# Kernel optimization log

Measured on AMD Instinct MI355X. Metric: run time of the kernel, lower is better.

The kernel has to match this reference:

```python
import jax, jax.numpy as jnp
import numpy as np

N, D = 4096, 512
TAU, ALPHA, EPS = 0.2, 0.5, 1e-15
L2_EPS = 1e-12  # F.normalize eps


def setup_inputs() -> dict:
    key = jax.random.key(0)
    ks = jax.random.split(key, 12)
    # xavier_normal_ with gain=1.414 for [D, D] linears
    std = 1.414 * (2.0 / (D + D)) ** 0.5
    xn = lambda k: jax.random.normal(k, (D, D), jnp.float32) * std
    return {
        "z1": jax.random.normal(ks[0], (N, D), jnp.float32),
        "z2": jax.random.normal(ks[1], (N, D), jnp.float32),
        # local projector: Linear -> PReLU -> Linear
        "lw1": xn(ks[2]), "lb1": jnp.zeros((D,), jnp.float32),
        "la": jnp.full((1,), 0.25, jnp.float32),  # PReLU weight (torch default 0.25)
        "lw2": xn(ks[3]), "lb2": jnp.zeros((D,), jnp.float32),
        # global projector
        "gw1": xn(ks[4]), "gb1": jnp.zeros((D,), jnp.float32),
        "ga": jnp.full((1,), 0.25, jnp.float32),
        "gw2": xn(ks[5]), "gb2": jnp.zeros((D,), jnp.float32),
        # discriminator bilinear weight
        "W": xn(ks[6]),
        # binary positive-pair mask [N, N]
        "mask": jax.random.randint(ks[7], (N, N), 0, 2, jnp.int32),
    }


def _prelu(x, a):
    return jnp.where(x >= 0, x, a * x)


def _proj(z, w1, b1, a, w2, b2):
    # nn.Sequential(Linear, PReLU, Linear); torch Linear: z @ W.T + b
    return _prelu(z @ w1.T + b1, a[0]) @ w2.T + b2


def _l2norm(z):
    n = jnp.linalg.norm(z, axis=-1, keepdims=True)
    return z / jnp.maximum(n, L2_EPS)


def _infonce(h1, h2, m, tau):
    a = _l2norm(h1)
    b = _l2norm(h2)
    sim_intra = jnp.exp(a @ a.T / tau)  # [N, N]
    sim_inter = jnp.exp(a @ b.T / tau)  # [N, N]
    num = (sim_inter * m).sum(1)
    den = sim_intra.sum(1) + sim_inter.sum(1) - (sim_intra * m).sum(1)
    return (-jnp.log(num / den)).mean()


def reference(z1, z2, lw1, lb1, la, lw2, lb2, gw1, gb1, ga, gw2, gb2, W, mask):
    m = mask.astype(jnp.float32)
    # local (node-level) InfoNCE through the local projector
    h1 = _proj(z1, lw1, lb1, la, lw2, lb2)
    h2 = _proj(z2, lw1, lb1, la, lw2, lb2)
    local = 0.5 * (_infonce(h1, h2, m, TAU) + _infonce(h2, h1, m.T, TAU))

    # global (DGI-style) loss
    def gloss(pos_z, neg_z):
        s = pos_z.mean(0)                               # readout [D]
        h = _proj(s, gw1, gb1, ga, gw2, gb2)            # global projector [D]
        summ = W @ h                                    # [D]
        d_pos = jax.nn.sigmoid(pos_z @ summ)            # [N]
        d_neg = jax.nn.sigmoid(neg_z @ summ)            # [N]
        pos_loss = -jnp.log(d_pos + EPS).mean()
        neg_loss = -jnp.log(1.0 - d_neg + EPS).mean()
        return 0.5 * (pos_loss + neg_loss)

    glob = 0.5 * (gloss(z1, z2) + gloss(z2, z1))
    return ALPHA * local + (1.0 - ALPHA) * glob
```

## Files before the change

### kernel.cpp

```cpp
#include <hip/hip_runtime.h>
#include <math.h>

#define NN 4096
#define DD 512
#define INV_TAU 5.0f
#define EPSV 1e-15f

typedef unsigned short u16;
typedef __attribute__((ext_vector_type(8))) short short8;
typedef __attribute__((ext_vector_type(4))) float f32x4;

__device__ __forceinline__ void gld16(const void* g, void* l) {
  __builtin_amdgcn_global_load_lds(
      (const __attribute__((address_space(1))) unsigned int*)g,
      (__attribute__((address_space(3))) unsigned int*)l, 16, 0, 0);
}

__device__ __forceinline__ void bar_vm4() {
  asm volatile("s_waitcnt vmcnt(4) lgkmcnt(0)\n\ts_barrier" ::: "memory");
}
__device__ __forceinline__ void bar_vm0() {
  asm volatile("s_waitcnt vmcnt(0) lgkmcnt(0)\n\ts_barrier" ::: "memory");
}

__device__ __forceinline__ float bf2f(u16 u) {
  return __uint_as_float(((unsigned)u) << 16);
}
__device__ __forceinline__ u16 f2bf(float x) {
  unsigned u = __float_as_uint(x);
  u += 0x7fff + ((u >> 16) & 1);
  return (u16)(u >> 16);
}

__device__ __forceinline__ float wave_sum(float v) {
#pragma unroll
  for (int o = 32; o > 0; o >>= 1) v += __shfl_down(v, o, 64);
  return v;
}

__global__ __launch_bounds__(256) void tobf16_2(const float* __restrict__ a,
                                                const float* __restrict__ b,
                                                u16* __restrict__ d,
                                                int n4each) {
  const int i = blockIdx.x * 256 + threadIdx.x;
  const float* s =
      (i < n4each) ? a + (size_t)i * 4 : b + (size_t)(i - n4each) * 4;
  float4 v = *(const float4*)s;
  unsigned long long pk = (unsigned long long)f2bf(v.x) |
                          ((unsigned long long)f2bf(v.y) << 16) |
                          ((unsigned long long)f2bf(v.z) << 32) |
                          ((unsigned long long)f2bf(v.w) << 48);
  *(unsigned long long*)&d[(size_t)i * 4] = pk;
}

template <int ACT>
__global__ __launch_bounds__(256) void gemm_mfma(
    const u16* __restrict__ A, const u16* __restrict__ Bw,
    const float* __restrict__ bias, const float* __restrict__ alpha_p,
    u16* __restrict__ out) {
  __shared__ __align__(16) u16 sh[3 * 2 * 128 * 32];
  const int tid = threadIdx.x, w = tid >> 6, lane = tid & 63;
  const int quad = lane >> 4, m16 = lane & 15;
  const int wi = w >> 1, wj = w & 1;
  const int i0 = blockIdx.y * 128, j0 = blockIdx.x * 128;
  const u16* Ab = A + (size_t)blockIdx.z * ((size_t)NN * DD);
  u16* ob = out + (size_t)blockIdx.z * ((size_t)NN * DD);
  const int roff =
      (m16 >> 1) * 64 + (((((m16 & 1) << 2) | quad) ^ (m16 >> 1)) * 8);
  const int st = (lane & 7) ^ (lane >> 3);
  const int srow = 2 * (lane >> 3) + (st >> 2);
  const int scol = (st & 3) * 8;
  const int p = w >> 1, rh = (w & 1) * 64;
  const u16* gs = p ? Bw : Ab;
  const int gr = (p ? j0 : i0) + rh + srow;
  u16* dst0 = sh + p * 4096 + rh * 32;
  auto stage = [&](int bo, int k) {
    const int kn = k * 32;
#pragma unroll
    for (int rr = 0; rr < 64; rr += 16)
      gld16(&gs[(size_t)(gr + rr) * DD + kn + scol], dst0 + bo + rr * 32);
  };
  stage(0, 0);
  stage(8192, 1);
  bar_vm4();
  f32x4 acc[4][4] = {};
  int ro = 0;
  for (int kc = 0; kc < 16; ++kc) {
    if (kc <= 13) {
      int so = ro + 16384;
      if (so >= 24576) so -= 24576;
      stage(so, kc + 2);
    }
    const u16* As = sh + ro;
    const u16* Bs = sh + ro + 4096;
    short8 ar[4], br[4];
#pragma unroll
    for (int s = 0; s < 4; ++s) {
      ar[s] = *(const short8*)&As[(wi * 64 + s * 16) * 32 + roff];
      br[s] = *(const short8*)&Bs[(wj * 64 + s * 16) * 32 + roff];
    }
    __builtin_amdgcn_s_setprio(1);
#pragma unroll
    for (int si = 0; si < 4; ++si)
#pragma unroll
      for (int sj = 0; sj < 4; ++sj)
        acc[si][sj] = __builtin_amdgcn_mfma_f32_16x16x32_bf16(
            ar[si], br[sj], acc[si][sj], 0, 0, 0);
    __builtin_amdgcn_s_setprio(0);
    if (kc <= 13) bar_vm4();
    else if (kc == 14) bar_vm0();
    ro += 8192;
    if (ro == 24576) ro = 0;
  }
  const float al = ACT ? alpha_p[0] : 0.f;
#pragma unroll
  for (int si = 0; si < 4; ++si)
#pragma unroll
    for (int sj = 0; sj < 4; ++sj) {
      const int col = j0 + wj * 64 + sj * 16 + m16;
      const float bv = bias[col];
#pragma unroll
      for (int r = 0; r < 4; ++r) {
        const int row = i0 + wi * 64 + si * 16 + quad * 4 + r;
        float x = acc[si][sj][r] + bv;
        if (ACT) x = (x >= 0.f) ? x : al * x;
        ob[(size_t)row * DD + col] = f2bf(x);
      }
    }
}

__global__ __launch_bounds__(256) void rownorm_bf16(const u16* __restrict__ h,
                                                    u16* __restrict__ o) {
  const int row = blockIdx.x;
  const int t = threadIdx.x;
  const size_t base = (size_t)row * DD;
  float v0 = bf2f(h[base + t]);
  float v1 = bf2f(h[base + 256 + t]);
  float s = v0 * v0 + v1 * v1;
  s = wave_sum(s);
  __shared__ float wsum[4];
  const int lane = t & 63, wid = t >> 6;
  if (lane == 0) wsum[wid] = s;
  __syncthreads();
  if (t == 0) {
    float tot = wsum[0] + wsum[1] + wsum[2] + wsum[3];
    wsum[0] = 1.f / fmaxf(sqrtf(tot), 1e-12f);
  }
  __syncthreads();
  const float inv = wsum[0];
  o[base + t] = f2bf(v0 * inv);
  o[base + 256 + t] = f2bf(v1 * inv);
}

__global__ __launch_bounds__(512) void sim_mfma(
    const u16* __restrict__ na, const u16* __restrict__ nb,
    const int* __restrict__ mask, float* __restrict__ zb) {
  extern __shared__ __align__(16) u16 shm[];
  const int tid = threadIdx.x;
  const int w = tid >> 6, lane = tid & 63;
  const int quad = lane >> 4, m16 = lane & 15;
  const int ig = w & 3, jh = w >> 2;
  const int i0 = blockIdx.y * 128, j0 = blockIdx.x * 128;
  const int roff =
      (m16 >> 1) * 64 + (((((m16 & 1) << 2) | quad) ^ (m16 >> 1)) * 8);
  const int st = (lane & 7) ^ (lane >> 3);
  const int srow = 2 * (lane >> 3) + (st >> 2);
  const int scol = (st & 3) * 8;
  const int p = w >> 1, rh = (w & 1) * 64;
  const u16* gs = (p & 1) ? nb : na;
  const int gr = ((p < 2) ? i0 : j0) + rh + srow;
  u16* dst0 = shm + p * 4096 + rh * 32;
  auto stage = [&](int bo, int k) {
    const int kn = k * 32;
#pragma unroll
    for (int rr = 0; rr < 64; rr += 16)
      gld16(&gs[(size_t)(gr + rr) * DD + kn + scol], dst0 + bo + rr * 32);
  };
  stage(0, 0);
  stage(16384, 1);
  bar_vm4();
  f32x4 a11[2][4] = {}, a12[2][4] = {}, a22[2][4] = {};
  int ro = 0;
  for (int kc = 0; kc < 16; ++kc) {
    if (kc <= 13) {
      int so = ro + 32768;
      if (so >= 49152) so -= 49152;
      stage(so, kc + 2);
    }
    const u16* Ai = shm + ro;
    const u16* Bi = shm + ro + 4096;
    const u16* Aj = shm + ro + 8192;
    const u16* Bj = shm + ro + 12288;
    short8 ai0 = *(const short8*)&Ai[(ig * 32) * 32 + roff];
    short8 ai1 = *(const short8*)&Ai[(ig * 32 + 16) * 32 + roff];
    short8 bi0 = *(const short8*)&Bi[(ig * 32) * 32 + roff];
    short8 bi1 = *(const short8*)&Bi[(ig * 32 + 16) * 32 + roff];
#pragma unroll
    for (int c = 0; c < 4; ++c) {
      short8 aj = *(const short8*)&Aj[(jh * 64 + c * 16) * 32 + roff];
      short8 bj = *(const short8*)&Bj[(jh * 64 + c * 16) * 32 + roff];
      __builtin_amdgcn_s_setprio(1);
      a11[0][c] = __builtin_amdgcn_mfma_f32_16x16x32_bf16(ai0, aj, a11[0][c], 0, 0, 0);
      a11[1][c] = __builtin_amdgcn_mfma_f32_16x16x32_bf16(ai1, aj, a11[1][c], 0, 0, 0);
      a12[0][c] = __builtin_amdgcn_mfma_f32_16x16x32_bf16(ai0, bj, a12[0][c], 0, 0, 0);
      a12[1][c] = __builtin_amdgcn_mfma_f32_16x16x32_bf16(ai1, bj, a12[1][c], 0, 0, 0);
      a22[0][c] = __builtin_amdgcn_mfma_f32_16x16x32_bf16(bi0, bj, a22[0][c], 0, 0, 0);
      a22[1][c] = __builtin_amdgcn_mfma_f32_16x16x32_bf16(bi1, bj, a22[1][c], 0, 0, 0);
      __builtin_amdgcn_s_setprio(0);
    }
    if (kc <= 13) bar_vm4();
    else if (kc == 14) bar_vm0();
    ro += 16384;
    if (ro == 49152) ro = 0;
  }
  float* rred = (float*)(shm + 16384);
  float* cred = rred + 512;
  rred[tid] = 0.f;
  rred[tid + 512] = 0.f;
  __syncthreads();
  float rs11[2][4] = {}, rm11[2][4] = {}, rs12[2][4] = {}, rm12[2][4] = {};
  float cs12[4] = {}, cm12[4] = {}, cs22[4] = {}, cm22[4] = {};
#pragma unroll
  for (int t = 0; t < 2; ++t)
#pragma unroll
    for (int c = 0; c < 4; ++c) {
      const int gj = j0 + jh * 64 + c * 16 + m16;
#pragma unroll
      for (int r = 0; r < 4; ++r) {
        const int gi = i0 + ig * 32 + t * 16 + quad * 4 + r;
        const float mv = (float)mask[(size_t)gi * NN + gj];
        const float e11 = __expf(a11[t][c][r] * INV_TAU);
        const float e12 = __expf(a12[t][c][r] * INV_TAU);
        const float e22 = __expf(a22[t][c][r] * INV_TAU);
        rs11[t][r] += e11;
        rm11[t][r] += e11 * mv;
        rs12[t][r] += e12;
        rm12[t][r] += e12 * mv;
        cs12[c] += e12;
        cm12[c] += e12 * mv;
        cs22[c] += e22;
        cm22[c] += e22 * mv;
      }
    }
#pragma unroll
  for (int t = 0; t < 2; ++t)
#pragma unroll
    for (int r = 0; r < 4; ++r) {
      float v0 = rs11[t][r], v1 = rm11[t][r], v2 = rs12[t][r], v3 = rm12[t][r];
#pragma unroll
      for (int o = 1; o < 16; o <<= 1) {
        v0 += __shfl_xor(v0, o, 64);
        v1 += __shfl_xor(v1, o, 64);
        v2 += __shfl_xor(v2, o, 64);
        v3 += __shfl_xor(v3, o, 64);
      }
      if (m16 == 0) {
        const int il = ig * 32 + t * 16 + quad * 4 + r;
        atomicAdd(&rred[0 * 128 + il], v0);
        atomicAdd(&rred[1 * 128 + il], v1);
        atomicAdd(&rred[2 * 128 + il], v2);
        atomicAdd(&rred[3 * 128 + il], v3);
      }
    }
#pragma unroll
  for (int c = 0; c < 4; ++c) {
    float v0 = cs12[c], v1 = cm12[c], v2 = cs22[c], v3 = cm22[c];
    v0 += __shfl_xor(v0, 16, 64); v0 += __shfl_xor(v0, 32, 64);
    v1 += __shfl_xor(v1, 16, 64); v1 += __shfl_xor(v1, 32, 64);
    v2 += __shfl_xor(v2, 16, 64); v2 += __shfl_xor(v2, 32, 64);
    v3 += __shfl_xor(v3, 16, 64); v3 += __shfl_xor(v3, 32, 64);
    if (lane < 16) {
      const int jl = jh * 64 + c * 16 + lane;
      atomicAdd(&cred[0 * 128 + jl], v0);
      atomicAdd(&cred[1 * 128 + jl], v1);
      atomicAdd(&cred[2 * 128 + jl], v2);
      atomicAdd(&cred[3 * 128 + jl], v3);
    }
  }
  __syncthreads();
  if (tid < 128) {
#pragma unroll
    for (int q = 0; q < 4; ++q)
      atomicAdd(&zb[q * NN + i0 + tid], rred[q * 128 + tid]);
  } else if (tid < 256) {
    const int jl = tid - 128;
#pragma unroll
    for (int q = 0; q < 4; ++q)
      atomicAdd(&zb[(4 + q) * NN + j0 + jl], cred[q * 128 + jl]);
  }
}

__global__ __launch_bounds__(256) void local_fin(const float* __restrict__ zb,
                                                 float* __restrict__ scal) {
  const int i = blockIdx.x * 256 + threadIdx.x;
  const float r11 = zb[i], r11m = zb[NN + i];
  const float r12 = zb[2 * NN + i], r12m = zb[3 * NN + i];
  const float c12 = zb[4 * NN + i], c12m = zb[5 * NN + i];
  const float c22 = zb[6 * NN + i], c22m = zb[7 * NN + i];
  float l1 = -logf(r12m / (r11 + r12 - r11m));
  float l2 = -logf(c12m / (c22 + c12 - c22m));
  l1 = wave_sum(l1);
  l2 = wave_sum(l2);
  __shared__ float b1[4], b2[4];
  const int lane = threadIdx.x & 63, wid = threadIdx.x >> 6;
  if (lane == 0) { b1[wid] = l1; b2[wid] = l2; }
  __syncthreads();
  if (threadIdx.x == 0) {
    atomicAdd(&scal[0], b1[0] + b1[1] + b1[2] + b1[3]);
    atomicAdd(&scal[1], b2[0] + b2[1] + b2[2] + b2[3]);
  }
}

__global__ __launch_bounds__(256) void colmean(const float* __restrict__ z1,
                                               const float* __restrict__ z2,
                                               float* __restrict__ s1,
                                               float* __restrict__ s2) {
  const int c = blockIdx.x * 256 + threadIdx.x;
  const int r0 = blockIdx.y * 64;
  float a = 0.f, b = 0.f;
  for (int r = r0; r < r0 + 64; ++r) {
    a += z1[(size_t)r * DD + c];
    b += z2[(size_t)r * DD + c];
  }
  atomicAdd(&s1[c], a * (1.f / NN));
  atomicAdd(&s2[c], b * (1.f / NN));
}

__global__ __launch_bounds__(256) void matvec2(
    const float* __restrict__ M, const float* __restrict__ x1,
    const float* __restrict__ x2, const float* __restrict__ bias,
    const float* __restrict__ alpha_p, int act, float* __restrict__ y1,
    float* __restrict__ y2) {
  const float* x = blockIdx.y ? x2 : x1;
  float* y = blockIdx.y ? y2 : y1;
  const int row = (blockIdx.x * 256 + threadIdx.x) >> 6;
  const int lane = threadIdx.x & 63;
  float acc = 0.f;
#pragma unroll
  for (int t = 0; t < 8; ++t)
    acc = fmaf(M[(size_t)row * DD + lane + 64 * t], x[lane + 64 * t], acc);
  acc = wave_sum(acc);
  if (lane == 0) {
    if (bias) acc += bias[row];
    if (act) { const float al = alpha_p[0]; acc = (acc >= 0.f) ? acc : al * acc; }
    y[row] = acc;
  }
}

__global__ __launch_bounds__(256) void logsig2(
    const float* __restrict__ z1, const float* __restrict__ z2,
    const float* __restrict__ sm1, const float* __restrict__ sm2,
    float* __restrict__ scal) {
  const int ch = blockIdx.y;
  const float* z = ch ? z2 : z1;
  const float* sp = ch ? sm2 : sm1;
  const float* sn = ch ? sm1 : sm2;
  float* accP = ch ? &scal[4] : &scal[2];
  float* accN = ch ? &scal[3] : &scal[5];
  const int lane = threadIdx.x & 63;
  const int wid = threadIdx.x >> 6;
  const int row = blockIdx.x * 4 + wid;
  float dp = 0.f, dn = 0.f;
#pragma unroll
  for (int t = 0; t < 8; ++t) {
    const float zv = z[(size_t)row * DD + lane + 64 * t];
    dp = fmaf(zv, sp[lane + 64 * t], dp);
    dn = fmaf(zv, sn[lane + 64 * t], dn);
  }
  dp = wave_sum(dp);
  dn = wave_sum(dn);
  __shared__ float bp[4], bn[4];
  if (lane == 0) {
    const float sg = 1.f / (1.f + __expf(-dp));
    bp[wid] = -logf(sg + EPSV);
    const float sg2 = 1.f / (1.f + __expf(-dn));
    bn[wid] = -logf(1.f - sg2 + EPSV);
  }
  __syncthreads();
  if (threadIdx.x == 0) {
    atomicAdd(accP, bp[0] + bp[1] + bp[2] + bp[3]);
    atomicAdd(accN, bn[0] + bn[1] + bn[2] + bn[3]);
  }
}

__global__ void combine(const float* __restrict__ scal, float* __restrict__ out) {
  const float local = 0.5f * (scal[0] + scal[1]) * (1.f / NN);
  const float glob = 0.25f * (scal[2] + scal[3] + scal[4] + scal[5]) * (1.f / NN);
  out[0] = 0.5f * local + 0.5f * glob;
}

extern "C" void kernel_launch(void* const* d_in, const int* in_sizes, int n_in,
                              void* d_out, int out_size, void* d_ws,
                              size_t ws_size, hipStream_t stream) {
  const float* z1 = (const float*)d_in[0];
  const float* z2 = (const float*)d_in[1];
  const float* lw1 = (const float*)d_in[2];
  const float* lb1 = (const float*)d_in[3];
  const float* la = (const float*)d_in[4];
  const float* lw2 = (const float*)d_in[5];
  const float* lb2 = (const float*)d_in[6];
  const float* gw1 = (const float*)d_in[7];
  const float* gb1 = (const float*)d_in[8];
  const float* ga = (const float*)d_in[9];
  const float* gw2 = (const float*)d_in[10];
  const float* gb2 = (const float*)d_in[11];
  const float* W = (const float*)d_in[12];
  const int* mask = (const int*)d_in[13];
  float* out = (float*)d_out;

  static bool attr_set = false;
  if (!attr_set) {
    (void)hipFuncSetAttribute(reinterpret_cast<const void*>(sim_mfma),
                              hipFuncAttributeMaxDynamicSharedMemorySize,
                              98304);
    attr_set = true;
  }

  const size_t ND = (size_t)NN * DD;
  u16* W1b = (u16*)d_ws;
  u16* W2b = W1b + 512 * 512;
  u16* Ab = W1b + 2 * 512 * 512;
  u16* Bb = Ab + 2 * ND;
  float* zbf = (float*)(Bb + 2 * ND);
  float* s1 = zbf + 8 * NN;
  float* s2 = s1 + DD;
  float* scal = s2 + DD;
  float* t1 = scal + 16;
  float* hg1 = t1 + DD;
  float* summ1 = hg1 + DD;
  float* t2 = summ1 + DD;
  float* hg2 = t2 + DD;
  float* summ2 = hg2 + DD;

  hipMemsetAsync(zbf, 0, (8 * NN + 2 * DD + 16) * sizeof(float), stream);

  dim3 blk(256);
  tobf16_2<<<512, blk, 0, stream>>>(lw1, lw2, W1b, 512 * 512 / 4);
  tobf16_2<<<4096, blk, 0, stream>>>(z1, z2, Ab, (int)(ND / 4));

  dim3 gg(4, 32, 2);
  gemm_mfma<1><<<gg, blk, 0, stream>>>(Ab, W1b, lb1, la, Bb);
  gemm_mfma<0><<<gg, blk, 0, stream>>>(Bb, W2b, lb2, la, Ab);
  rownorm_bf16<<<2 * NN, blk, 0, stream>>>(Ab, Bb);

  sim_mfma<<<dim3(NN / 128, NN / 128), dim3(512), 98304, stream>>>(
      Bb, Bb + ND, mask, zbf);
  local_fin<<<NN / 256, blk, 0, stream>>>(zbf, scal);

  colmean<<<dim3(DD / 256, 64), blk, 0, stream>>>(z1, z2, s1, s2);
  matvec2<<<dim3(DD / 4, 2), blk, 0, stream>>>(gw1, s1, s2, gb1, ga, 1, t1, t2);
  matvec2<<<dim3(DD / 4, 2), blk, 0, stream>>>(gw2, t1, t2, gb2, nullptr, 0, hg1, hg2);
  matvec2<<<dim3(DD / 4, 2), blk, 0, stream>>>(W, hg1, hg2, nullptr, nullptr, 0, summ1, summ2);
  logsig2<<<dim3(NN / 4, 2), blk, 0, stream>>>(z1, z2, summ1, summ2, scal);

  combine<<<1, 1, 0, stream>>>(scal, out);
}
```

Before: 310.2 us.

## Fuse pipeline: merged conversion/colsum, GEMM+rownorm, single matvec chain, last-block finalize

Replaces most of the launch sequence. The bf16 conversion of weights and z, the zeroing of accumulators and the column partial sums now run in one kernel. The first GEMM gets a 512-thread, XCD-aware 128x64 tiling, and the second GEMM is fused with L2 row normalization over full-width 32-row bands. The three global matvecs become one 2-block kernel, and the loss finalize and combine run in the last sim_mfma block via an atomic counter. This removes the memset, several launches and intermediate round-trips through memory, at the cost of a serial single-block tail and low parallelism in mv_chain.

```diff
diff --git a/kernel.cpp b/kernel.cpp
--- a/kernel.cpp
+++ b/kernel.cpp
@@ -16,8 +16,17 @@
       (__attribute__((address_space(3))) unsigned int*)l, 16, 0, 0);
 }
 
+__device__ __forceinline__ void bar_vm5() {
+  asm volatile("s_waitcnt vmcnt(5) lgkmcnt(0)\n\ts_barrier" ::: "memory");
+}
 __device__ __forceinline__ void bar_vm4() {
   asm volatile("s_waitcnt vmcnt(4) lgkmcnt(0)\n\ts_barrier" ::: "memory");
+}
+__device__ __forceinline__ void bar_vm2() {
+  asm volatile("s_waitcnt vmcnt(2) lgkmcnt(0)\n\ts_barrier" ::: "memory");
+}
+__device__ __forceinline__ void bar_vm1() {
+  asm volatile("s_waitcnt vmcnt(1) lgkmcnt(0)\n\ts_barrier" ::: "memory");
 }
 __device__ __forceinline__ void bar_vm0() {
   asm volatile("s_waitcnt vmcnt(0) lgkmcnt(0)\n\ts_barrier" ::: "memory");
@@ -38,123 +47,382 @@
   return v;
 }
 
-__global__ __launch_bounds__(256) void tobf16_2(const float* __restrict__ a,
-                                                const float* __restrict__ b,
-                                                u16* __restrict__ d,
-                                                int n4each) {
-  const int i = blockIdx.x * 256 + threadIdx.x;
-  const float* s =
-      (i < n4each) ? a + (size_t)i * 4 : b + (size_t)(i - n4each) * 4;
+__device__ __forceinline__ float ldz(const float* p) {
+  return __hip_atomic_load(p, __ATOMIC_RELAXED, __HIP_MEMORY_SCOPE_AGENT);
+}
+
+__global__ __launch_bounds__(256) void tobf16cm(
+    const float* __restrict__ a, const float* __restrict__ b,
+    const float* __restrict__ c, const float* __restrict__ d2,
+    u16* __restrict__ o, float* __restrict__ pc1, float* __restrict__ pc2,
+    float* __restrict__ zbf, int* __restrict__ ctr) {
+  const int bid = blockIdx.x, tid = threadIdx.x;
+  if (bid >= 4608) {
+    const int blk = bid - 4608;
+    const int r0 = blk * 32;
+    float a0 = 0.f, a1 = 0.f, c0 = 0.f, c1 = 0.f;
+    for (int r = r0; r < r0 + 32; ++r) {
+      const size_t ro = (size_t)r * DD;
+      a0 += c[ro + tid];
+      a1 += c[ro + 256 + tid];
+      c0 += d2[ro + tid];
+      c1 += d2[ro + 256 + tid];
+    }
+    pc1[blk * 512 + tid] = a0;
+    pc1[blk * 512 + 256 + tid] = a1;
+    pc2[blk * 512 + tid] = c0;
+    pc2[blk * 512 + 256 + tid] = c1;
+    return;
+  }
+  if (bid == 0 && tid == 0) ctr[0] = 0;
+  if (bid < 128) zbf[bid * 256 + tid] = 0.f;
+  const int i = bid * 256 + tid;
+  int j = i;
+  const float* s;
+  if (j < 65536) {
+    s = a + (size_t)j * 4;
+  } else {
+    j -= 65536;
+    if (j < 65536) {
+      s = b + (size_t)j * 4;
+    } else {
+      j -= 65536;
+      if (j < 524288) {
+        s = c + (size_t)j * 4;
+      } else {
+        j -= 524288;
+        s = d2 + (size_t)j * 4;
+      }
+    }
+  }
   float4 v = *(const float4*)s;
   unsigned long long pk = (unsigned long long)f2bf(v.x) |
                           ((unsigned long long)f2bf(v.y) << 16) |
                           ((unsigned long long)f2bf(v.z) << 32) |
                           ((unsigned long long)f2bf(v.w) << 48);
-  *(unsigned long long*)&d[(size_t)i * 4] = pk;
+  *(unsigned long long*)&o[(size_t)i * 4] = pk;
 }
 
 template <int ACT>
-__global__ __launch_bounds__(256) void gemm_mfma(
+__global__ __launch_bounds__(512) void gemm_mfma(
     const u16* __restrict__ A, const u16* __restrict__ Bw,
     const float* __restrict__ bias, const float* __restrict__ alpha_p,
     u16* __restrict__ out) {
-  __shared__ __align__(16) u16 sh[3 * 2 * 128 * 32];
+  __shared__ __align__(16) u16 sh[3 * 6144];
   const int tid = threadIdx.x, w = tid >> 6, lane = tid & 63;
   const int quad = lane >> 4, m16 = lane & 15;
   const int wi = w >> 1, wj = w & 1;
-  const int i0 = blockIdx.y * 128, j0 = blockIdx.x * 128;
-  const u16* Ab = A + (size_t)blockIdx.z * ((size_t)NN * DD);
-  u16* ob = out + (size_t)blockIdx.z * ((size_t)NN * DD);
+  const int bid = blockIdx.x;
+  const int xcd = bid & 7, idx = bid >> 3;
+  const int i0 = (4 * xcd + (idx & 3)) * 128;
+  const int j0 = ((idx >> 2) & 7) * 64;
+  const int bz = idx >> 5;
+  const u16* Ab = A + (size_t)bz * ((size_t)NN * DD);
+  u16* ob = out + (size_t)bz * ((size_t)NN * DD);
   const int roff =
       (m16 >> 1) * 64 + (((((m16 & 1) << 2) | quad) ^ (m16 >> 1)) * 8);
   const int st = (lane & 7) ^ (lane >> 3);
   const int srow = 2 * (lane >> 3) + (st >> 2);
   const int scol = (st & 3) * 8;
-  const int p = w >> 1, rh = (w & 1) * 64;
-  const u16* gs = p ? Bw : Ab;
-  const int gr = (p ? j0 : i0) + rh + srow;
-  u16* dst0 = sh + p * 4096 + rh * 32;
+  const u16* gs = (w < 4) ? Ab : Bw;
+  const int grow0 = ((w < 4) ? i0 + 2 * w * 16 : j0 + (w - 4) * 16) + srow;
+  const int doff0 = (w < 4) ? 2 * w * 512 : 4096 + (w - 4) * 512;
   auto stage = [&](int bo, int k) {
     const int kn = k * 32;
-#pragma unroll
-    for (int rr = 0; rr < 64; rr += 16)
-      gld16(&gs[(size_t)(gr + rr) * DD + kn + scol], dst0 + bo + rr * 32);
+    gld16(&gs[(size_t)grow0 * DD + kn + scol], sh + bo + doff0);
+    if (w < 4)
+      gld16(&gs[(size_t)(grow0 + 16) * DD + kn + scol], sh + bo + doff0 + 512);
   };
   stage(0, 0);
-  stage(8192, 1);
-  bar_vm4();
-  f32x4 acc[4][4] = {};
+  stage(6144, 1);
+  if (w < 4) bar_vm2(); else bar_vm1();
+  f32x4 acc[2][2] = {};
   int ro = 0;
   for (int kc = 0; kc < 16; ++kc) {
     if (kc <= 13) {
-      int so = ro + 16384;
-      if (so >= 24576) so -= 24576;
+      int so = ro + 12288;
+      if (so >= 18432) so -= 18432;
       stage(so, kc + 2);
     }
     const u16* As = sh + ro;
     const u16* Bs = sh + ro + 4096;
-    short8 ar[4], br[4];
-#pragma unroll
-    for (int s = 0; s < 4; ++s) {
-      ar[s] = *(const short8*)&As[(wi * 64 + s * 16) * 32 + roff];
-      br[s] = *(const short8*)&Bs[(wj * 64 + s * 16) * 32 + roff];
+    short8 ar[2], br[2];
+#pragma unroll
+    for (int s = 0; s < 2; ++s) {
+      ar[s] = *(const short8*)&As[(wi * 32 + s * 16) * 32 + roff];
+      br[s] = *(const short8*)&Bs[(wj * 32 + s * 16) * 32 + roff];
     }
     __builtin_amdgcn_s_setprio(1);
 #pragma unroll
-    for (int si = 0; si < 4; ++si)
+    for (int si = 0; si < 2; ++si)
+#pragma unroll
+      for (int sj = 0; sj < 2; ++sj)
+        acc[si][sj] = __builtin_amdgcn_mfma_f32_16x16x32_bf16(
+            ar[si], br[sj], acc[si][sj], 0, 0, 0);
+    __builtin_amdgcn_s_setprio(0);
+    if (kc <= 13) {
+      if (w < 4) bar_vm2(); else bar_vm1();
+    } else if (kc == 14) {
+      bar_vm0();
+    }
+    ro += 6144;
+    if (ro == 18432) ro = 0;
+  }
+  const float al = ACT ? alpha_p[0] : 0.f;
+#pragma unroll
+  for (int si = 0; si < 2; ++si)
+#pragma unroll
+    for (int sj = 0; sj < 2; ++sj) {
+      const int col = j0 + wj * 32 + sj * 16 + m16;
+      const float bv = bias[col];
+#pragma unroll
+      for (int r = 0; r < 4; ++r) {
+        const int row = i0 + wi * 32 + si * 16 + quad * 4 + r;
+        float x = acc[si][sj][r] + bv;
+        if (ACT) x = (x >= 0.f) ? x : al * x;
+        ob[(size_t)row * DD + col] = f2bf(x);
+      }
+    }
+}
+
+__global__ __launch_bounds__(512) void gemm2n(const u16* __restrict__ Ain,
+                                              const u16* __restrict__ Bw,
+                                              const float* __restrict__ bias,
+                                              u16* __restrict__ outn) {
+  extern __shared__ __align__(16) u16 shb[];
+  const int BUF = 17408;
+  const int tid = threadIdx.x, w = tid >> 6, lane = tid & 63;
+  const int quad = lane >> 4, m16 = lane & 15;
+  const int bid = blockIdx.x;
+  const int bz = bid >> 7, band = bid & 127;
+  const int i0 = band * 32;
+  const u16* Ab = Ain + (size_t)bz * ((size_t)NN * DD);
+  u16* ob = outn + (size_t)bz * ((size_t)NN * DD);
+  const int roff =
+      (m16 >> 1) * 64 + (((((m16 & 1) << 2) | quad) ^ (m16 >> 1)) * 8);
+  const int st = (lane & 7) ^ (lane >> 3);
+  const int srow = 2 * (lane >> 3) + (st >> 2);
+  const int scol = (st & 3) * 8;
+  const int g0 = w * 4;
+  auto stage = [&](int bo, int k) {
+    const int kn = k * 32;
+#pragma unroll
+    for (int q = 0; q < 4; ++q) {
+      const int grow = (g0 + q) * 16 + srow;
+      gld16(&Bw[(size_t)grow * DD + kn + scol], shb + bo + (g0 + q) * 512);
+    }
+    if (w < 2) {
+      const int grow = i0 + w * 16 + srow;
+      gld16(&Ab[(size_t)grow * DD + kn + scol], shb + bo + 16384 + w * 512);
+    }
+  };
+  stage(0, 0);
+  stage(BUF, 1);
+  if (w < 2) bar_vm5(); else bar_vm4();
+  f32x4 acc[2][4] = {};
+  int ro = 0;
+  for (int kc = 0; kc < 16; ++kc) {
+    if (kc <= 13) {
+      int so = ro + 2 * BUF;
+      if (so >= 3 * BUF) so -= 3 * BUF;
+      stage(so, kc + 2);
+    }
+    const u16* Bs = shb + ro;
+    const u16* As = shb + ro + 16384;
+    short8 ar[2], br[4];
+#pragma unroll
+    for (int s = 0; s < 2; ++s)
+      ar[s] = *(const short8*)&As[(s * 16) * 32 + roff];
+#pragma unroll
+    for (int s = 0; s < 4; ++s)
+      br[s] = *(const short8*)&Bs[(w * 64 + s * 16) * 32 + roff];
+    __builtin_amdgcn_s_setprio(1);
+#pragma unroll
+    for (int si = 0; si < 2; ++si)
 #pragma unroll
       for (int sj = 0; sj < 4; ++sj)
         acc[si][sj] = __builtin_amdgcn_mfma_f32_16x16x32_bf16(
             ar[si], br[sj], acc[si][sj], 0, 0, 0);
     __builtin_amdgcn_s_setprio(0);
-    if (kc <= 13) bar_vm4();
-    else if (kc == 14) bar_vm0();
-    ro += 8192;
-    if (ro == 24576) ro = 0;
-  }
-  const float al = ACT ? alpha_p[0] : 0.f;
-#pragma unroll
-  for (int si = 0; si < 4; ++si)
+    if (kc <= 13) {
+      if (w < 2) bar_vm5(); else bar_vm4();
+    } else if (kc == 14) {
+      bar_vm0();
+    }
+    ro += BUF;
+    if (ro == 3 * BUF) ro = 0;
+  }
+  float ss[2][4] = {};
+#pragma unroll
+  for (int si = 0; si < 2; ++si)
 #pragma unroll
     for (int sj = 0; sj < 4; ++sj) {
-      const int col = j0 + wj * 64 + sj * 16 + m16;
-      const float bv = bias[col];
+      const float bv = bias[w * 64 + sj * 16 + m16];
 #pragma unroll
       for (int r = 0; r < 4; ++r) {
-        const int row = i0 + wi * 64 + si * 16 + quad * 4 + r;
-        float x = acc[si][sj][r] + bv;
-        if (ACT) x = (x >= 0.f) ? x : al * x;
-        ob[(size_t)row * DD + col] = f2bf(x);
+        const float x = acc[si][sj][r] + bv;
+        acc[si][sj][r] = x;
+        ss[si][r] = fmaf(x, x, ss[si][r]);
       }
     }
-}
-
-__global__ __launch_bounds__(256) void rownorm_bf16(const u16* __restrict__ h,
-                                                    u16* __restrict__ o) {
-  const int row = blockIdx.x;
-  const int t = threadIdx.x;
-  const size_t base = (size_t)row * DD;
-  float v0 = bf2f(h[base + t]);
-  float v1 = bf2f(h[base + 256 + t]);
-  float s = v0 * v0 + v1 * v1;
-  s = wave_sum(s);
-  __shared__ float wsum[4];
-  const int lane = t & 63, wid = t >> 6;
-  if (lane == 0) wsum[wid] = s;
-  __syncthreads();
-  if (t == 0) {
-    float tot = wsum[0] + wsum[1] + wsum[2] + wsum[3];
-    wsum[0] = 1.f / fmaxf(sqrtf(tot), 1e-12f);
-  }
-  __syncthreads();
-  const float inv = wsum[0];
-  o[base + t] = f2bf(v0 * inv);
-  o[base + 256 + t] = f2bf(v1 * inv);
+#pragma unroll
+  for (int si = 0; si < 2; ++si)
+#pragma unroll
+    for (int r = 0; r < 4; ++r) {
+#pragma unroll
+      for (int o = 1; o < 16; o <<= 1) ss[si][r] += __shfl_xor(ss[si][r], o, 64);
+    }
+  float* part = (float*)(shb + BUF);
+  float* invn = part + 256;
+  if (m16 == 0) {
+#pragma unroll
+    for (int si = 0; si < 2; ++si)
+#pragma unroll
+      for (int r = 0; r < 4; ++r)
+        part[(si * 16 + quad * 4 + r) * 8 + w] = ss[si][r];
+  }
+  __syncthreads();
+  if (tid < 32) {
+    float s = 0.f;
+#pragma unroll
+    for (int q = 0; q < 8; ++q) s += part[tid * 8 + q];
+    invn[tid] = 1.f / fmaxf(sqrtf(s), 1e-12f);
+  }
+  __syncthreads();
+#pragma unroll
+  for (int si = 0; si < 2; ++si)
+#pragma unroll
+    for (int sj = 0; sj < 4; ++sj) {
+      const int col = w * 64 + sj * 16 + m16;
+#pragma unroll
+      for (int r = 0; r < 4; ++r) {
+        const int r32 = si * 16 + quad * 4 + r;
+        ob[(size_t)(i0 + r32) * DD + col] = f2bf(acc[si][sj][r] * invn[r32]);
+      }
+    }
+}
+
+__global__ __launch_bounds__(1024) void mv_chain(
+    const float* __restrict__ pc1, const float* __restrict__ pc2,
+    const float* __restrict__ gw1, const float* __restrict__ gb1,
+    const float* __restrict__ ga, const float* __restrict__ gw2,
+    const float* __restrict__ gb2, const float* __restrict__ W,
+    float* __restrict__ summ1, float* __restrict__ summ2) {
+  const int bz = blockIdx.x;
+  const float* pc = bz ? pc2 : pc1;
+  float* summ = bz ? summ2 : summ1;
+  __shared__ float sv[512], tv[512], hv[512];
+  const int tid = threadIdx.x;
+  if (tid < 512) {
+    float a = 0.f;
+    for (int b = 0; b < 128; ++b) a += pc[b * 512 + tid];
+    sv[tid] = a * (1.f / NN);
+  }
+  __syncthreads();
+  const int w = tid >> 6, lane = tid & 63;
+  for (int rq = 0; rq < 8; ++rq) {
+    const int row = w * 32 + rq * 4;
+    float a0 = 0.f, a1 = 0.f, a2 = 0.f, a3 = 0.f;
+#pragma unroll
+    for (int t = 0; t < 8; ++t) {
+      const float x = sv[lane + 64 * t];
+      a0 = fmaf(gw1[(size_t)(row + 0) * DD + lane + 64 * t], x, a0);
+      a1 = fmaf(gw1[(size_t)(row + 1) * DD + lane + 64 * t], x, a1);
+      a2 = fmaf(gw1[(size_t)(row + 2) * DD + lane + 64 * t], x, a2);
+      a3 = fmaf(gw1[(size_t)(row + 3) * DD + lane + 64 * t], x, a3);
+    }
+    a0 = wave_sum(a0); a1 = wave_sum(a1); a2 = wave_sum(a2); a3 = wave_sum(a3);
+    if (lane == 0) {
+      const float al = ga[0];
+      float v0 = a0 + gb1[row + 0], v1 = a1 + gb1[row + 1];
+      float v2 = a2 + gb1[row + 2], v3 = a3 + gb1[row + 3];
+      tv[row + 0] = (v0 >= 0.f) ? v0 : al * v0;
+      tv[row + 1] = (v1 >= 0.f) ? v1 : al * v1;
+      tv[row + 2] = (v2 >= 0.f) ? v2 : al * v2;
+      tv[row + 3] = (v3 >= 0.f) ? v3 : al * v3;
+    }
+  }
+  __syncthreads();
+  for (int rq = 0; rq < 8; ++rq) {
+    const int row = w * 32 + rq * 4;
+    float a0 = 0.f, a1 = 0.f, a2 = 0.f, a3 = 0.f;
+#pragma unroll
+    for (int t = 0; t < 8; ++t) {
+      const float x = tv[lane + 64 * t];
+      a0 = fmaf(gw2[(size_t)(row + 0) * DD + lane + 64 * t], x, a0);
+      a1 = fmaf(gw2[(size_t)(row + 1) * DD + lane + 64 * t], x, a1);
+      a2 = fmaf(gw2[(size_t)(row + 2) * DD + lane + 64 * t], x, a2);
+      a3 = fmaf(gw2[(size_t)(row + 3) * DD + lane + 64 * t], x, a3);
+    }
+    a0 = wave_sum(a0); a1 = wave_sum(a1); a2 = wave_sum(a2); a3 = wave_sum(a3);
+    if (lane == 0) {
+      hv[row + 0] = a0 + gb2[row + 0];
+      hv[row + 1] = a1 + gb2[row + 1];
+      hv[row + 2] = a2 + gb2[row + 2];
+      hv[row + 3] = a3 + gb2[row + 3];
+    }
+  }
+  __syncthreads();
+  for (int rq = 0; rq < 8; ++rq) {
+    const int row = w * 32 + rq * 4;
+    float a0 = 0.f, a1 = 0.f, a2 = 0.f, a3 = 0.f;
+#pragma unroll
+    for (int t = 0; t < 8; ++t) {
+      const float x = hv[lane + 64 * t];
+      a0 = fmaf(W[(size_t)(row + 0) * DD + lane + 64 * t], x, a0);
+      a1 = fmaf(W[(size_t)(row + 1) * DD + lane + 64 * t], x, a1);
+      a2 = fmaf(W[(size_t)(row + 2) * DD + lane + 64 * t], x, a2);
+      a3 = fmaf(W[(size_t)(row + 3) * DD + lane + 64 * t], x, a3);
+    }
+    a0 = wave_sum(a0); a1 = wave_sum(a1); a2 = wave_sum(a2); a3 = wave_sum(a3);
+    if (lane == 0) {
+      summ[row + 0] = a0;
+      summ[row + 1] = a1;
+      summ[row + 2] = a2;
+      summ[row + 3] = a3;
+    }
+  }
+}
+
+__global__ __launch_bounds__(256) void logsigp(
+    const float* __restrict__ z1, const float* __restrict__ z2,
+    const float* __restrict__ sm1, const float* __restrict__ sm2,
+    float* __restrict__ plsP, float* __restrict__ plsN) {
+  const int ch = blockIdx.y;
+  const float* z = ch ? z2 : z1;
+  const float* sp = ch ? sm2 : sm1;
+  const float* sn = ch ? sm1 : sm2;
+  const int lane = threadIdx.x & 63;
+  const int wid = threadIdx.x >> 6;
+  const int row = blockIdx.x * 4 + wid;
+  float dp = 0.f, dn = 0.f;
+#pragma unroll
+  for (int t = 0; t < 8; ++t) {
+    const float zv = z[(size_t)row * DD + lane + 64 * t];
+    dp = fmaf(zv, sp[lane + 64 * t], dp);
+    dn = fmaf(zv, sn[lane + 64 * t], dn);
+  }
+  dp = wave_sum(dp);
+  dn = wave_sum(dn);
+  __shared__ float bp[4], bn[4];
+  if (lane == 0) {
+    const float sg = 1.f / (1.f + __expf(-dp));
+    bp[wid] = -logf(sg + EPSV);
+    const float sg2 = 1.f / (1.f + __expf(-dn));
+    bn[wid] = -logf(1.f - sg2 + EPSV);
+  }
+  __syncthreads();
+  if (threadIdx.x == 0) {
+    plsP[ch * 1024 + blockIdx.x] = bp[0] + bp[1] + bp[2] + bp[3];
+    plsN[ch * 1024 + blockIdx.x] = bn[0] + bn[1] + bn[2] + bn[3];
+  }
 }
 
 __global__ __launch_bounds__(512) void sim_mfma(
     const u16* __restrict__ na, const u16* __restrict__ nb,
-    const int* __restrict__ mask, float* __restrict__ zb) {
+    const int* __restrict__ mask, float* __restrict__ zb,
+    int* __restrict__ ctr, const float* __restrict__ plsP,
+    const float* __restrict__ plsN, float* __restrict__ out) {
   extern __shared__ __align__(16) u16 shm[];
   const int tid = threadIdx.x;
   const int w = tid >> 6, lane = tid & 63;
@@ -288,105 +556,43 @@
     for (int q = 0; q < 4; ++q)
       atomicAdd(&zb[(4 + q) * NN + j0 + jl], cred[q * 128 + jl]);
   }
-}
-
-__global__ __launch_bounds__(256) void local_fin(const float* __restrict__ zb,
-                                                 float* __restrict__ scal) {
-  const int i = blockIdx.x * 256 + threadIdx.x;
-  const float r11 = zb[i], r11m = zb[NN + i];
-  const float r12 = zb[2 * NN + i], r12m = zb[3 * NN + i];
-  const float c12 = zb[4 * NN + i], c12m = zb[5 * NN + i];
-  const float c22 = zb[6 * NN + i], c22m = zb[7 * NN + i];
-  float l1 = -logf(r12m / (r11 + r12 - r11m));
-  float l2 = -logf(c12m / (c22 + c12 - c22m));
-  l1 = wave_sum(l1);
-  l2 = wave_sum(l2);
-  __shared__ float b1[4], b2[4];
-  const int lane = threadIdx.x & 63, wid = threadIdx.x >> 6;
-  if (lane == 0) { b1[wid] = l1; b2[wid] = l2; }
-  __syncthreads();
-  if (threadIdx.x == 0) {
-    atomicAdd(&scal[0], b1[0] + b1[1] + b1[2] + b1[3]);
-    atomicAdd(&scal[1], b2[0] + b2[1] + b2[2] + b2[3]);
-  }
-}
-
-__global__ __launch_bounds__(256) void colmean(const float* __restrict__ z1,
-                                               const float* __restrict__ z2,
-                                               float* __restrict__ s1,
-                                               float* __restrict__ s2) {
-  const int c = blockIdx.x * 256 + threadIdx.x;
-  const int r0 = blockIdx.y * 64;
-  float a = 0.f, b = 0.f;
-  for (int r = r0; r < r0 + 64; ++r) {
-    a += z1[(size_t)r * DD + c];
-    b += z2[(size_t)r * DD + c];
-  }
-  atomicAdd(&s1[c], a * (1.f / NN));
-  atomicAdd(&s2[c], b * (1.f / NN));
-}
-
-__global__ __launch_bounds__(256) void matvec2(
-    const float* __restrict__ M, const float* __restrict__ x1,
-    const float* __restrict__ x2, const float* __restrict__ bias,
-    const float* __restrict__ alpha_p, int act, float* __restrict__ y1,
-    float* __restrict__ y2) {
-  const float* x = blockIdx.y ? x2 : x1;
-  float* y = blockIdx.y ? y2 : y1;
-  const int row = (blockIdx.x * 256 + threadIdx.x) >> 6;
-  const int lane = threadIdx.x & 63;
-  float acc = 0.f;
-#pragma unroll
-  for (int t = 0; t < 8; ++t)
-    acc = fmaf(M[(size_t)row * DD + lane + 64 * t], x[lane + 64 * t], acc);
-  acc = wave_sum(acc);
-  if (lane == 0) {
-    if (bias) acc += bias[row];
-    if (act) { const float al = alpha_p[0]; acc = (acc >= 0.f) ? acc : al * acc; }
-    y[row] = acc;
-  }
-}
-
-__global__ __launch_bounds__(256) void logsig2(
-    const float* __restrict__ z1, const float* __restrict__ z2,
-    const float* __restrict__ sm1, const float* __restrict__ sm2,
-    float* __restrict__ scal) {
-  const int ch = blockIdx.y;
-  const float* z = ch ? z2 : z1;
-  const float* sp = ch ? sm2 : sm1;
-  const float* sn = ch ? sm1 : sm2;
-  float* accP = ch ? &scal[4] : &scal[2];
-  float* accN = ch ? &scal[3] : &scal[5];
-  const int lane = threadIdx.x & 63;
-  const int wid = threadIdx.x >> 6;
-  const int row = blockIdx.x * 4 + wid;
-  float dp = 0.f, dn = 0.f;
-#pragma unroll
-  for (int t = 0; t < 8; ++t) {
-    const float zv = z[(size_t)row * DD + lane + 64 * t];
-    dp = fmaf(zv, sp[lane + 64 * t], dp);
-    dn = fmaf(zv, sn[lane + 64 * t], dn);
-  }
-  dp = wave_sum(dp);
-  dn = wave_sum(dn);
-  __shared__ float bp[4], bn[4];
-  if (lane == 0) {
-    const float sg = 1.f / (1.f + __expf(-dp));
-    bp[wid] = -logf(sg + EPSV);
-    const float sg2 = 1.f / (1.f + __expf(-dn));
-    bn[wid] = -logf(1.f - sg2 + EPSV);
-  }
-  __syncthreads();
-  if (threadIdx.x == 0) {
-    atomicAdd(accP, bp[0] + bp[1] + bp[2] + bp[3]);
-    atomicAdd(accN, bn[0] + bn[1] + bn[2] + bn[3]);
-  }
-}
-
-__global__ void combine(const float* __restrict__ scal, float* __restrict__ out) {
-  const float local = 0.5f * (scal[0] + scal[1]) * (1.f / NN);
-  const float glob = 0.25f * (scal[2] + scal[3] + scal[4] + scal[5]) * (1.f / NN);
-  out[0] = 0.5f * local + 0.5f * glob;
+  __threadfence();
+  __syncthreads();
+  __shared__ int lastf_s;
+  if (tid == 0) lastf_s = (atomicAdd(ctr, 1) == 1023) ? 1 : 0;
+  __syncthreads();
+  if (!lastf_s) return;
+  __threadfence();
+  float S1 = 0.f, S2 = 0.f;
+#pragma unroll
+  for (int k = 0; k < 8; ++k) {
+    const int i = tid + k * 512;
+    const float r11 = ldz(&zb[i]), r11m = ldz(&zb[NN + i]);
+    const float r12 = ldz(&zb[2 * NN + i]), r12m = ldz(&zb[3 * NN + i]);
+    const float c12 = ldz(&zb[4 * NN + i]), c12m = ldz(&zb[5 * NN + i]);
+    const float c22 = ldz(&zb[6 * NN + i]), c22m = ldz(&zb[7 * NN + i]);
+    S1 += -logf(r12m / (r11 + r12 - r11m));
+    S2 += -logf(c12m / (c22 + c12 - c22m));
+  }
+  float G = plsP[tid] + plsP[tid + 512] + plsP[tid + 1024] + plsP[tid + 1536] +
+            plsN[tid] + plsN[tid + 512] + plsN[tid + 1024] + plsN[tid + 1536];
+  S1 = wave_sum(S1);
+  S2 = wave_sum(S2);
+  G = wave_sum(G);
+  __shared__ float fr[3][8];
+  if (lane == 0) { fr[0][w] = S1; fr[1][w] = S2; fr[2][w] = G; }
+  __syncthreads();
+  if (tid == 0) {
+    float s1t = 0.f, s2t = 0.f, gt = 0.f;
+    for (int q = 0; q < 8; ++q) {
+      s1t += fr[0][q];
+      s2t += fr[1][q];
+      gt += fr[2][q];
+    }
+    const float local = 0.5f * (s1t + s2t) * (1.f / NN);
+    const float glob = 0.25f * gt * (1.f / NN);
+    out[0] = 0.5f * local + 0.5f * glob;
+  }
 }
 
 extern "C" void kernel_launch(void* const* d_in, const int* in_sizes, int n_in,
@@ -413,6 +619,9 @@
     (void)hipFuncSetAttribute(reinterpret_cast<const void*>(sim_mfma),
                               hipFuncAttributeMaxDynamicSharedMemorySize,
                               98304);
+    (void)hipFuncSetAttribute(reinterpret_cast<const void*>(gemm2n),
+                              hipFuncAttributeMaxDynamicSharedMemorySize,
+                              104448);
     attr_set = true;
   }
 
@@ -422,36 +631,21 @@
   u16* Ab = W1b + 2 * 512 * 512;
   u16* Bb = Ab + 2 * ND;
   float* zbf = (float*)(Bb + 2 * ND);
-  float* s1 = zbf + 8 * NN;
-  float* s2 = s1 + DD;
-  float* scal = s2 + DD;
-  float* t1 = scal + 16;
-  float* hg1 = t1 + DD;
-  float* summ1 = hg1 + DD;
-  float* t2 = summ1 + DD;
-  float* hg2 = t2 + DD;
-  float* summ2 = hg2 + DD;
-
-  hipMemsetAsync(zbf, 0, (8 * NN + 2 * DD + 16) * sizeof(float), stream);
+  float* pc1 = zbf + 8 * NN;
+  float* pc2 = pc1 + 128 * 512;
+  float* summ1 = pc2 + 128 * 512;
+  float* summ2 = summ1 + 512;
+  float* plsP = summ2 + 512;
+  float* plsN = plsP + 2048;
+  int* ctr = (int*)(plsN + 2048);
 
   dim3 blk(256);
-  tobf16_2<<<512, blk, 0, stream>>>(lw1, lw2, W1b, 512 * 512 / 4);
-  tobf16_2<<<4096, blk, 0, stream>>>(z1, z2, Ab, (int)(ND / 4));
-
-  dim3 gg(4, 32, 2);
-  gemm_mfma<1><<<gg, blk, 0, stream>>>(Ab, W1b, lb1, la, Bb);
-  gemm_mfma<0><<<gg, blk, 0, stream>>>(Bb, W2b, lb2, la, Ab);
-  rownorm_bf16<<<2 * NN, blk, 0, stream>>>(Ab, Bb);
-
-  sim_mfma<<<dim3(NN / 128, NN / 128), dim3(512), 98304, stream>>>(
-      Bb, Bb + ND, mask, zbf);
-  local_fin<<<NN / 256, blk, 0, stream>>>(zbf, scal);
-
-  colmean<<<dim3(DD / 256, 64), blk, 0, stream>>>(z1, z2, s1, s2);
-  matvec2<<<dim3(DD / 4, 2), blk, 0, stream>>>(gw1, s1, s2, gb1, ga, 1, t1, t2);
-  matvec2<<<dim3(DD / 4, 2), blk, 0, stream>>>(gw2, t1, t2, gb2, nullptr, 0, hg1, hg2);
-  matvec2<<<dim3(DD / 4, 2), blk, 0, stream>>>(W, hg1, hg2, nullptr, nullptr, 0, summ1, summ2);
-  logsig2<<<dim3(NN / 4, 2), blk, 0, stream>>>(z1, z2, summ1, summ2, scal);
-
-  combine<<<1, 1, 0, stream>>>(scal, out);
-}
+  tobf16cm<<<4736, blk, 0, stream>>>(lw1, lw2, z1, z2, W1b, pc1, pc2, zbf, ctr);
+  gemm_mfma<1><<<512, dim3(512), 0, stream>>>(Ab, W1b, lb1, la, Bb);
+  gemm2n<<<256, dim3(512), 104448, stream>>>(Bb, W2b, lb2, Ab);
+  mv_chain<<<2, dim3(1024), 0, stream>>>(pc1, pc2, gw1, gb1, ga, gw2, gb2, W,
+                                         summ1, summ2);
+  logsigp<<<dim3(1024, 2), blk, 0, stream>>>(z1, z2, summ1, summ2, plsP, plsN);
+  sim_mfma<<<dim3(32, 32), dim3(512), 98304, stream>>>(Ab, Ab + ND, mask, zbf,
+                                                       ctr, plsP, plsN, out);
+}
```

After: 427.0 us. 1.38x slower.
